# Kernel optimization log

Hardware: AMD Instinct MI355X
Metric: run time of the kernel (lower is better)

The kernel has to match this reference:

```python
import jax, jax.numpy as jnp
import numpy as np

NEG_INF = -jnp.inf

def _swish(x):
    return x * jax.nn.sigmoid(x)

def setup_inputs() -> dict:
    key = jax.random.key(0)
    ks = jax.random.split(key, 16)
    B, N, D = 16, 512, 256
    L, H, HS, FF = 4, 8, 64, 1024
    s = 0.05  # weight scale to keep activations stable over 4 layers
    inp = {
        "X": jax.random.normal(ks[0], (B, N, D), jnp.float32),
        "dag": jax.random.randint(ks[1], (N, N), 0, 2, jnp.int32),
        "Wk": jax.random.normal(ks[2], (L, H, D, HS), jnp.float32) * s,
        "bk": jnp.zeros((L, H, HS), jnp.float32),
        "Wq": jax.random.normal(ks[3], (L, H, D, HS), jnp.float32) * s,
        "bq": jnp.zeros((L, H, HS), jnp.float32),
        "Wv": jax.random.normal(ks[4], (L, H, D, HS), jnp.float32) * s,
        "bv": jnp.zeros((L, H, HS), jnp.float32),
        "Wp": jax.random.normal(ks[5], (L, H * HS, D), jnp.float32) * s,
        "bp": jnp.zeros((L, D), jnp.float32),
        "W1": jax.random.normal(ks[6], (L, D, FF), jnp.float32) * s,
        "b1": jnp.zeros((L, FF), jnp.float32),
        "W2": jax.random.normal(ks[7], (L, FF, D), jnp.float32) * s,
        "b2": jnp.zeros((L, D), jnp.float32),
        "Wlm": jax.random.normal(ks[8], (D, D), jnp.float32) * s,
        "blm": jnp.zeros((D,), jnp.float32),
    }
    return inp

def _block(X, dT, Wk, bk, Wq, bq, Wv, bv, Wp, bp, W1, b1, W2, b2):
    # X: (B, n, D); dT: (n, n) transposed (possibly identity-augmented) DAG
    B, n, D = X.shape
    hs = Wk.shape[-1]
    K = _swish(jnp.einsum('bnd,hdk->bhnk', X, Wk) + bk[None, :, None, :])
    Q = _swish(jnp.einsum('bnd,hdk->bhnk', X, Wq) + bq[None, :, None, :])
    V = _swish(jnp.einsum('bnd,hdk->bhnk', X, Wv) + bv[None, :, None, :])
    S = jnp.einsum('bhik,bhjk->bhij', Q, K) / (hs ** 0.5)      # (B,H,n,n)
    Sp = dT[None, None] * jnp.einsum('im,bhmj->bhij', dT, S)   # dag.T * (dag.T @ S)
    masked = jnp.where(Sp == 0, NEG_INF, Sp)
    dead = jnp.all(masked == NEG_INF, axis=-1, keepdims=True)  # rows that would softmax to NaN
    P = jax.nn.softmax(jnp.where(dead, 0.0, masked), axis=-1)
    P = jnp.where(dead, 0.0, P)                                # NaN-row zeroing, as in torch code
    O = jnp.einsum('bhij,bhjk->bhik', P, V) + jnp.einsum('ij,bhjk->bhik', dT, V)
    O = O.transpose(0, 2, 1, 3).reshape(B, n, -1)              # concat heads
    mha = _swish(O @ Wp + bp)                                  # projection + swish (dropout=0)
    ff = _swish(mha @ W1 + b1) @ W2 + b2                       # FF: Linear-Swish-Linear
    return mha + ff

def reference(X, dag, Wk, bk, Wq, bq, Wv, bv, Wp, bp, W1, b1, W2, b2, Wlm, blm):
    dagf = jnp.clip(dag.astype(X.dtype), 0, 1)
    n = dagf.shape[0]
    eye = jnp.eye(n, dtype=X.dtype)
    L = Wk.shape[0]
    for l in range(L):
        d = dagf if l == 0 else jnp.clip(dagf + eye, 0, 1)  # modify_dag
        X = _block(X, d.T, Wk[l], bk[l], Wq[l], bq[l], Wv[l], bv[l],
                   Wp[l], bp[l], W1[l], b1[l], W2[l], b2[l])
    return X @ Wlm + blm  # lm_head
```

## Files before the change

### kernel.cpp

```cpp
#include <hip/hip_runtime.h>
#include <hip/hip_bf16.h>
#include <math.h>


typedef __attribute__((ext_vector_type(8))) short bf16x8;
typedef __attribute__((ext_vector_type(4))) float f32x4;
typedef unsigned long long u64;

#define NEG_INF (-__builtin_inff())

__device__ __forceinline__ short f2bf(float x) {
  unsigned u = __float_as_uint(x);
  return (short)((u + 0x7FFFu + ((u >> 16) & 1u)) >> 16);
}
__device__ __forceinline__ float bf2f(short h) {
  return __uint_as_float(((unsigned)(unsigned short)h) << 16);
}
__device__ __forceinline__ void split_bf(float x, short& hi, short& lo) {
  hi = f2bf(x); lo = f2bf(x - bf2f(hi));
}
__device__ __forceinline__ float swishf(float x) { return x / (1.0f + __expf(-x)); }
__device__ __forceinline__ f32x4 mfma16(bf16x8 a, bf16x8 b, f32x4 c) {
  return __builtin_amdgcn_mfma_f32_16x16x32_bf16(a, b, c, 0, 0, 0);
}
__device__ __forceinline__ void gload16(const void* g, void* l) {
  __builtin_amdgcn_global_load_lds(
      (const __attribute__((address_space(1))) void*)g,
      (__attribute__((address_space(3))) void*)l, 16, 0, 0);
}

template<int P>
__global__ __launch_bounds__(256)
void wsplit(const float* __restrict__ in, short* __restrict__ oh, short* __restrict__ ol,
            int R, int C, int zh, long outLS)
{
  __shared__ float T[64][65];
  const int z = blockIdx.z;
  const long zin = (long)z * R * C;
  const long zout = (long)(z / zh) * outLS + (long)(z % zh) * R * C;
  const int r0 = blockIdx.y << 6, c0 = blockIdx.x << 6;
  const int lc = threadIdx.x & 63, p = threadIdx.x >> 6;
#pragma unroll
  for (int q = 0; q < 16; ++q) {
    int rr = p + q * 4;
    T[rr][lc] = in[zin + (long)(r0 + rr) * C + c0 + lc];
  }
  __syncthreads();
#pragma unroll
  for (int q = 0; q < 16; ++q) {
    int cr = p + q * 4;
    float x = T[lc][cr];
    long off = zout + (long)(c0 + cr) * R + r0 + lc;
    short hi = f2bf(x);
    oh[off] = hi;
    if (P == 2) ol[off] = f2bf(x - bf2f(hi));
  }
}

__global__ __launch_bounds__(512)
void prep_dt(const int* __restrict__ dag, short* __restrict__ dt0, short* __restrict__ dt1,
             u64* __restrict__ bits0, u64* __restrict__ bits1)
{
  int i = blockIdx.x, j = threadIdx.x;
  bool v0 = dag[j * 512 + i] > 0;
  bool v1 = v0 || (i == j);
  const short one = (short)0x3F80;
  dt0[i * 512 + j] = v0 ? one : (short)0;
  dt1[i * 512 + j] = v1 ? one : (short)0;
  u64 b0 = __ballot(v0), b1 = __ballot(v1);
  if ((j & 63) == 0) { bits0[i * 8 + (j >> 6)] = b0; bits1[i * 8 + (j >> 6)] = b1; }
}

__global__ __launch_bounds__(256)
void prep_x(const float* __restrict__ X, short* __restrict__ Xh, short* __restrict__ Xl)
{
  int idx = blockIdx.x * 256 + threadIdx.x;
  short hi, lo; split_bf(X[idx], hi, lo);
  Xh[idx] = hi; Xl[idx] = lo;
}

__global__ __launch_bounds__(256)
void pack_kq(const float* __restrict__ bk, const float* __restrict__ bq,
             float* __restrict__ bkq)
{
  int t = blockIdx.x * 256 + threadIdx.x;
  if (t >= 4096) return;
  int l = t >> 10, r = t & 1023;
  bkq[t] = (r < 512) ? bk[l * 512 + r] : bq[l * 512 + r - 512];
}

template<int BM, int BN, int AP, int BP, int OM, int OP, bool ACT, bool BIAS, bool RES>
__global__ __launch_bounds__(256)
void gemm(const short* __restrict__ Ah, const short* __restrict__ Al,
          const short* __restrict__ BTh, const short* __restrict__ BTl,
          const float* __restrict__ bias,
          const short* __restrict__ ResH, const short* __restrict__ ResL,
          float* __restrict__ Cf, short* __restrict__ Ch, short* __restrict__ Cl,
          short* __restrict__ Ch2,
          int K, int ldb, int ldc, long sB, long sC)
{
  constexpr int MR = BM / 32, NR = BN / 32;
  constexpr int ABUF = BM * 32;
  constexpr int BBUF = BN * 32;
  constexpr int STG = AP * ABUF + BP * BBUF;
  constexpr int TSZ = (OM >= 2) ? BN * (BM + 8) : 0;
  constexpr int SM = (2 * STG > TSZ) ? 2 * STG : TSZ;
  __shared__ __align__(16) short smem[SM];

  const int z = blockIdx.z;
  const short* pBh = BTh + (long)z * sB;
  const short* pBl = BTl + (long)z * sB;
  const int n0 = blockIdx.x * BN, m0 = blockIdx.y * BM;
  const int tid = threadIdx.x, lane = tid & 63, w = tid >> 6, g = lane >> 4, c = lane & 15;
  const int wm = w >> 1, wn = w & 1;

  auto stage = [&](int bb, int k0) {
    short* LA = smem + bb * STG;
    short* LB = LA + AP * ABUF;
#pragma unroll
    for (int p = 0; p < AP; ++p) {
      const short* src = p ? Al : Ah;
#pragma unroll
      for (int t = 0; t < BM / 64; ++t) {
        int u = t * 256 + tid, gi = u / BM, row = u % BM;
        gload16(src + (long)(m0 + row) * K + k0 + gi * 8, LA + p * ABUF + u * 8);
      }
    }
#pragma unroll
    for (int p = 0; p < BP; ++p) {
      const short* src = p ? pBl : pBh;
#pragma unroll
      for (int t = 0; t < BN / 64; ++t) {
        int u = t * 256 + tid, gi = u / BN, col = u % BN;
        gload16(src + (long)(n0 + col) * ldb + k0 + gi * 8, LB + p * BBUF + u * 8);
      }
    }
  };

  f32x4 acc[MR][NR] = {};
  stage(0, 0);
  const int nk = K >> 5;
  for (int ks = 0; ks < nk; ++ks) {
    const int cur = ks & 1;
    __syncthreads();
    if (ks + 1 < nk) stage(cur ^ 1, (ks + 1) << 5);

    short* LA = smem + cur * STG;
    short* LB = LA + AP * ABUF;
    bf16x8 a_h[MR], a_l[MR], b_h[NR], b_l[NR];
#pragma unroll
    for (int i = 0; i < MR; ++i) {
      int idx = (g * BM + wm * (BM / 2) + i * 16 + c) * 8;
      a_h[i] = *(const bf16x8*)(LA + idx);
      if (AP == 2) a_l[i] = *(const bf16x8*)(LA + ABUF + idx);
    }
#pragma unroll
    for (int j = 0; j < NR; ++j) {
      int idx = (g * BN + wn * (BN / 2) + j * 16 + c) * 8;
      b_h[j] = *(const bf16x8*)(LB + idx);
      if (BP == 2) b_l[j] = *(const bf16x8*)(LB + BBUF + idx);
    }
    __builtin_amdgcn_s_setprio(1);
#pragma unroll
    for (int i = 0; i < MR; ++i)
#pragma unroll
      for (int j = 0; j < NR; ++j) {
        acc[i][j] = mfma16(a_h[i], b_h[j], acc[i][j]);
        if (BP == 2) acc[i][j] = mfma16(a_h[i], b_l[j], acc[i][j]);
        if (AP == 2) acc[i][j] = mfma16(a_l[i], b_h[j], acc[i][j]);
      }
    __builtin_amdgcn_s_setprio(0);
  }

  const bool kq_rowmajor = (OM == 3) && (n0 < 512);
  if (OM == 0 || OM == 1 || kq_rowmajor) {
#pragma unroll
    for (int j = 0; j < NR; ++j) {
      int cl = wn * (BN / 2) + j * 16 + c;
      float bv = BIAS ? bias[n0 + cl] : 0.f;
      int col = (OM == 3) ? ((n0 & 511) + cl) : (n0 + cl);
#pragma unroll
      for (int i = 0; i < MR; ++i)
#pragma unroll
        for (int rr = 0; rr < 4; ++rr) {
          long row = m0 + wm * (BM / 2) + i * 16 + g * 4 + rr;
          float x = acc[i][j][rr] + bv;
          if (ACT) x = swishf(x);
          long off = (long)z * sC + row * ldc + col;
          if (RES) x += bf2f(ResH[off]) + bf2f(ResL[off]);
          if (OM == 1) { Cf[off] = x; }
          else {
            short hi, lo; split_bf(x, hi, lo);
            Ch[off] = hi;
            if (OM == 0 && OP == 2) Cl[off] = lo;
          }
        }
    }
    return;
  }

  if constexpr (OM >= 2) {
    short (*T)[BM + 8] = reinterpret_cast<short(*)[BM + 8]>(smem);
    const int h0 = (n0 & 511) >> 6;
    const int b = m0 >> 9, nn0 = m0 & 511;
    constexpr int NP = (OM == 3) ? 1 : OP;
#pragma unroll
    for (int p = 0; p < NP; ++p) {
      __syncthreads();
#pragma unroll
      for (int j = 0; j < NR; ++j) {
        int cl = wn * (BN / 2) + j * 16 + c;
        float bv = BIAS ? bias[n0 + cl] : 0.f;
#pragma unroll
        for (int i = 0; i < MR; ++i)
#pragma unroll
          for (int rr = 0; rr < 4; ++rr) {
            int rowl = wm * (BM / 2) + i * 16 + g * 4 + rr;
            float x = acc[i][j][rr] + bv;
            if (ACT) x = swishf(x);
            short hi = f2bf(x);
            T[cl][rowl] = p ? f2bf(x - bf2f(hi)) : hi;
          }
      }
      __syncthreads();
      short* dp = (OM == 3) ? Ch2 : (p ? Cl : Ch);
#pragma unroll
      for (int q = 0; q < BN * BM / 2048; ++q) {
        int idx = q * 256 + tid;
        int cl = idx / (BM / 8), r8 = (idx % (BM / 8)) * 8;
        long ob = ((long)(b * 8 + h0 + (cl >> 6)) << 15) + (long)(cl & 63) * 512 + nn0 + r8;
        *(bf16x8*)(dp + ob) = *(const bf16x8*)&T[cl][r8];
      }
    }
  }
}

__global__ __launch_bounds__(256)
void attn3(const short* __restrict__ Uh, const short* __restrict__ Kh,
           const short* __restrict__ VTh, const u64* __restrict__ bits,
           const float* __restrict__ OIf,
           short* __restrict__ Oh, short* __restrict__ Ol)
{
  __shared__ __align__(16) short LK[2][4096];
  __shared__ __align__(16) short LV[2][4096];
  __shared__ __align__(16) short PA[4][1024];

  const int bh = blockIdx.x, b = bh >> 3, hd = bh & 7;
  const int i0 = blockIdx.y << 6;
  const int tid = threadIdx.x, lane = tid & 63, w = tid >> 6, g = lane >> 4, c = lane & 15;
  const int istrip = i0 + w * 16;
  const long plane = (long)bh << 15;
  const float SC = 0.125f;

  auto stage = [&](int bb, int jt) {
#pragma unroll
    for (int t = 0; t < 2; ++t) {
      int u = t * 256 + tid, gi = u >> 6, j = u & 63;
      long ko = (long)(b * 512 + jt * 64 + j) * 512 + hd * 64 + gi * 8;
      gload16(Kh + ko, &LK[bb][0] + u * 8);
      long vo = plane + (long)j * 512 + jt * 64 + gi * 8;
      gload16(VTh + vo, &LV[bb][0] + u * 8);
    }
  };

  stage(0, 0);

  bf16x8 ufh[2];
#pragma unroll
  for (int ks = 0; ks < 2; ++ks)
    ufh[ks] = *(const bf16x8*)(Uh + plane + (long)(istrip + c) * 64 + ks * 32 + g * 8);

  float m_run[4], l_run[4];
#pragma unroll
  for (int rr = 0; rr < 4; ++rr) { m_run[rr] = NEG_INF; l_run[rr] = 0.f; }
  f32x4 oe[4] = {};

  for (int jt = 0; jt < 8; ++jt) {
    const int cur = jt & 1;
    __syncthreads();
    if (jt + 1 < 8) stage(cur ^ 1, jt + 1);

    f32x4 sacc[4] = {};
    __builtin_amdgcn_s_setprio(1);
#pragma unroll
    for (int ct = 0; ct < 4; ++ct)
#pragma unroll
      for (int ks = 0; ks < 2; ++ks) {
        bf16x8 kf = *(const bf16x8*)&LK[cur][((ks * 4 + g) * 64 + ct * 16 + c) * 8];
        sacc[ct] = mfma16(ufh[ks], kf, sacc[ct]);
      }
    __builtin_amdgcn_s_setprio(0);

    u64 wb[4];
#pragma unroll
    for (int rr = 0; rr < 4; ++rr)
      wb[rr] = bits[(long)(istrip + g * 4 + rr) * 8 + jt];

#pragma unroll
    for (int rr = 0; rr < 4; ++rr) {
      float vmax = NEG_INF;
#pragma unroll
      for (int ct = 0; ct < 4; ++ct)
        if ((wb[rr] >> (ct * 16 + c)) & 1ull) vmax = fmaxf(vmax, sacc[ct][rr] * SC);
#pragma unroll
      for (int off = 1; off < 16; off <<= 1)
        vmax = fmaxf(vmax, __shfl_xor(vmax, off, 64));
      float mnew = fmaxf(m_run[rr], vmax);
      float sf = (m_run[rr] > NEG_INF) ? __expf(m_run[rr] - mnew) : 0.f;
      float ps = 0.f, p[4];
#pragma unroll
      for (int ct = 0; ct < 4; ++ct) {
        bool bs = (wb[rr] >> (ct * 16 + c)) & 1ull;
        p[ct] = (bs && mnew > NEG_INF) ? __expf(sacc[ct][rr] * SC - mnew) : 0.f;
        ps += p[ct];
      }
#pragma unroll
      for (int off = 1; off < 16; off <<= 1)
        ps += __shfl_xor(ps, off, 64);
      l_run[rr] = l_run[rr] * sf + ps;
      m_run[rr] = mnew;
#pragma unroll
      for (int ct = 0; ct < 4; ++ct) {
        oe[ct][rr] *= sf;
        int row = g * 4 + rr, jc = ct * 16 + c;
        PA[w][row * 64 + (((jc >> 3) ^ (row & 7)) << 3) + (c & 7)] = f2bf(p[ct]);
      }
    }

    __builtin_amdgcn_s_setprio(1);
#pragma unroll
    for (int js = 0; js < 2; ++js) {
      int chunk = js * 4 + g;
      bf16x8 pa = *(const bf16x8*)&PA[w][c * 64 + ((chunk ^ (c & 7)) << 3)];
#pragma unroll
      for (int ct = 0; ct < 4; ++ct) {
        bf16x8 vf = *(const bf16x8*)&LV[cur][((js * 4 + g) * 64 + ct * 16 + c) * 8];
        oe[ct] = mfma16(pa, vf, oe[ct]);
      }
    }
    __builtin_amdgcn_s_setprio(0);
  }

  float rl[4];
#pragma unroll
  for (int rr = 0; rr < 4; ++rr) rl[rr] = (l_run[rr] > 0.f) ? 1.f / l_run[rr] : 0.f;
#pragma unroll
  for (int ct = 0; ct < 4; ++ct)
#pragma unroll
    for (int rr = 0; rr < 4; ++rr) {
      int n = istrip + g * 4 + rr;
      int hs = ct * 16 + c;
      float x = oe[ct][rr] * rl[rr] + OIf[plane + (long)n * 64 + hs];
      long row = (long)b * 512 + n;
      short hi, lo; split_bf(x, hi, lo);
      Oh[row * 512 + hd * 64 + hs] = hi;
      Ol[row * 512 + hd * 64 + hs] = lo;
    }
}

extern "C" void kernel_launch(void* const* d_in, const int* in_sizes, int n_in,
                              void* d_out, int out_size, void* d_ws, size_t ws_size,
                              hipStream_t stream)
{
  const float* X   = (const float*)d_in[0];
  const int*   dag = (const int*)d_in[1];
  const float* Wk  = (const float*)d_in[2];
  const float* bk  = (const float*)d_in[3];
  const float* Wq  = (const float*)d_in[4];
  const float* bq  = (const float*)d_in[5];
  const float* Wv  = (const float*)d_in[6];
  const float* bv  = (const float*)d_in[7];
  const float* Wp  = (const float*)d_in[8];
  const float* bp  = (const float*)d_in[9];
  const float* W1  = (const float*)d_in[10];
  const float* b1  = (const float*)d_in[11];
  const float* W2  = (const float*)d_in[12];
  const float* b2  = (const float*)d_in[13];
  const float* Wlm = (const float*)d_in[14];
  const float* blm = (const float*)d_in[15];
  float* out = (float*)d_out;

  char* p = (char*)d_ws;
  auto alloc = [&](size_t n) { void* r = p; p += (n + 255) & ~(size_t)255; return r; };
  short* WkqTh = (short*)alloc(1048576 * 2);
  short* WvTh = (short*)alloc(524288 * 2); short* WvTl = (short*)alloc(524288 * 2);
  short* WpTh = (short*)alloc(524288 * 2); short* WpTl = (short*)alloc(524288 * 2);
  short* W1Th = (short*)alloc(1048576 * 2); short* W1Tl = (short*)alloc(1048576 * 2);
  short* W2Th = (short*)alloc(1048576 * 2); short* W2Tl = (short*)alloc(1048576 * 2);
  short* WlmTh = (short*)alloc(65536 * 2); short* WlmTl = (short*)alloc(65536 * 2);
  float* bkq = (float*)alloc(4096 * 4);
  short* dt0b = (short*)alloc(262144 * 2); short* dt1b = (short*)alloc(262144 * 2);
  u64* bits0 = (u64*)alloc(4096 * 8); u64* bits1 = (u64*)alloc(4096 * 8);
  short* Xh = (short*)alloc(2097152 * 2); short* Xl = (short*)alloc(2097152 * 2);
  short* Kh = (short*)alloc(4194304 * 2);
  short* QTh = (short*)alloc(4194304 * 2);
  short* VTh = (short*)alloc(4194304 * 2); short* VTl = (short*)alloc(4194304 * 2);
  short* Uh  = (short*)alloc(4194304 * 2);
  float* OIf = (float*)alloc(4194304 * 4);
  short* Olo = (short*)alloc(4194304 * 2);
  short* mhaH = Kh, *mhaL = Kh + 2097152;
  short* Oh = QTh;
  short* ff1H = VTh;
  short* ff1L = Uh;

  wsplit<1><<<dim3(1, 4, 32), 256, 0, stream>>>(Wk, WkqTh, nullptr, 256, 64, 8, 262144);
  wsplit<1><<<dim3(1, 4, 32), 256, 0, stream>>>(Wq, WkqTh + 131072, nullptr, 256, 64, 8, 262144);
  wsplit<2><<<dim3(1, 4, 32), 256, 0, stream>>>(Wv, WvTh, WvTl, 256, 64, 8, 131072);
  wsplit<2><<<dim3(4, 8, 4), 256, 0, stream>>>(Wp, WpTh, WpTl, 512, 256, 1, 131072);
  wsplit<2><<<dim3(16, 4, 4), 256, 0, stream>>>(W1, W1Th, W1Tl, 256, 1024, 1, 262144);
  wsplit<2><<<dim3(4, 16, 4), 256, 0, stream>>>(W2, W2Th, W2Tl, 1024, 256, 1, 262144);
  wsplit<2><<<dim3(4, 4, 1), 256, 0, stream>>>(Wlm, WlmTh, WlmTl, 256, 256, 1, 65536);
  prep_dt<<<512, 512, 0, stream>>>(dag, dt0b, dt1b, bits0, bits1);
  prep_x<<<8192, 256, 0, stream>>>(X, Xh, Xl);
  pack_kq<<<16, 256, 0, stream>>>(bk, bq, bkq);

  for (int l = 0; l < 4; ++l) {
    const short* dtb = l ? dt1b : dt0b;
    const u64* bts = l ? bits1 : bits0;
    gemm<128, 64, 1, 1, 3, 1, true, true, false><<<dim3(16, 64), 256, 0, stream>>>(
        Xh, nullptr, WkqTh + l * 262144, nullptr, bkq + l * 1024, nullptr, nullptr,
        nullptr, Kh, nullptr, QTh, 256, 256, 512, 0, 0);
    gemm<128, 64, 2, 2, 2, 2, true, true, false><<<dim3(8, 64), 256, 0, stream>>>(
        Xh, Xl, WvTh + l * 131072, WvTl + l * 131072, bv + l * 512, nullptr, nullptr,
        nullptr, VTh, VTl, nullptr, 256, 256, 0, 0, 0);
    gemm<128, 64, 1, 1, 0, 1, false, false, false><<<dim3(1, 4, 128), 256, 0, stream>>>(
        dtb, nullptr, QTh, nullptr, nullptr, nullptr, nullptr,
        nullptr, Uh, nullptr, nullptr, 512, 512, 64, 32768, 32768);
    gemm<128, 64, 1, 2, 1, 1, false, false, false><<<dim3(1, 4, 128), 256, 0, stream>>>(
        dtb, nullptr, VTh, VTl, nullptr, nullptr, nullptr,
        OIf, nullptr, nullptr, nullptr, 512, 512, 64, 32768, 32768);
    attn3<<<dim3(128, 8), 256, 0, stream>>>(Uh, Kh, VTh, bts, OIf, Oh, Olo);
    gemm<64, 64, 2, 2, 0, 2, true, true, false><<<dim3(4, 128), 256, 0, stream>>>(
        Oh, Olo, WpTh + l * 131072, WpTl + l * 131072, bp + l * 256, nullptr, nullptr,
        nullptr, mhaH, mhaL, nullptr, 512, 512, 256, 0, 0);
    gemm<128, 64, 2, 2, 0, 2, true, true, false><<<dim3(16, 64), 256, 0, stream>>>(
        mhaH, mhaL, W1Th + l * 262144, W1Tl + l * 262144, b1 + l * 1024, nullptr, nullptr,
        nullptr, ff1H, ff1L, nullptr, 256, 256, 1024, 0, 0);
    gemm<64, 64, 2, 2, 0, 2, false, true, true><<<dim3(4, 128), 256, 0, stream>>>(
        ff1H, ff1L, W2Th + l * 262144, W2Tl + l * 262144, b2 + l * 256, mhaH, mhaL,
        nullptr, Xh, Xl, nullptr, 1024, 1024, 256, 0, 0);
  }
  gemm<64, 64, 2, 2, 1, 1, false, true, false><<<dim3(4, 128), 256, 0, stream>>>(
      Xh, Xl, WlmTh, WlmTl, blm, nullptr, nullptr,
      out, nullptr, nullptr, nullptr, 256, 256, 256, 0, 0);
}
```

Measured before the change: 916.4 us.

## Rewrite attention with transposed register softmax and drop low-precision splits for V/Wp

Attention now computes S transposed so each lane owns one query row, keeping the softmax in registers and feeding P to the PV MFMA through cross-lane shuffles instead of an LDS staging buffer. The 1/sqrt(hs) scale is folded into the Q epilogue. V and Wp lose their low-bf16 halves and the attention output is written as a single bf16, which cuts MFMA and memory work but lowers precision. The identity-term GEMM is recast as a transposed batched GEMM, and the row-major GEMM epilogues now stage through LDS to issue vectorised 16-byte stores.

```diff
diff --git a/kernel.cpp b/kernel.cpp
--- a/kernel.cpp
+++ b/kernel.cpp
@@ -27,6 +27,11 @@
   __builtin_amdgcn_global_load_lds(
       (const __attribute__((address_space(1))) void*)g,
       (__attribute__((address_space(3))) void*)l, 16, 0, 0);
+}
+__device__ __forceinline__ unsigned cvtpk(float a, float b) {
+  unsigned r;
+  asm("v_cvt_pk_bf16_f32 %0, %1, %2" : "=v"(r) : "v"(a), "v"(b));
+  return r;
 }
 
 template<int P>
@@ -97,17 +102,20 @@
           const short* __restrict__ ResH, const short* __restrict__ ResL,
           float* __restrict__ Cf, short* __restrict__ Ch, short* __restrict__ Cl,
           short* __restrict__ Ch2,
-          int K, int ldb, int ldc, long sB, long sC)
+          int K, int ldb, int ldc, long sA, long sB, long sC)
 {
   constexpr int MR = BM / 32, NR = BN / 32;
-  constexpr int ABUF = BM * 32;
-  constexpr int BBUF = BN * 32;
+  constexpr int ABUF = BM * 32, BBUF = BN * 32;
   constexpr int STG = AP * ABUF + BP * BBUF;
-  constexpr int TSZ = (OM >= 2) ? BN * (BM + 8) : 0;
-  constexpr int SM = (2 * STG > TSZ) ? 2 * STG : TSZ;
+  constexpr int TSZ2 = (OM == 2 || OM == 3) ? BN * (BM + 8) : 0;
+  constexpr int TSZF = (OM == 0 || OM == 3) ? BM * (BN + 4) * 2 : 0;
+  constexpr int SM1 = (2 * STG > TSZ2) ? 2 * STG : TSZ2;
+  constexpr int SM = (SM1 > TSZF) ? SM1 : TSZF;
   __shared__ __align__(16) short smem[SM];
 
   const int z = blockIdx.z;
+  const short* pAh = Ah + (long)z * sA;
+  const short* pAl = Al + (long)z * sA;
   const short* pBh = BTh + (long)z * sB;
   const short* pBl = BTl + (long)z * sB;
   const int n0 = blockIdx.x * BN, m0 = blockIdx.y * BM;
@@ -119,7 +127,7 @@
     short* LB = LA + AP * ABUF;
 #pragma unroll
     for (int p = 0; p < AP; ++p) {
-      const short* src = p ? Al : Ah;
+      const short* src = p ? pAl : pAh;
 #pragma unroll
       for (int t = 0; t < BM / 64; ++t) {
         int u = t * 256 + tid, gi = u / BM, row = u % BM;
@@ -172,13 +180,11 @@
     __builtin_amdgcn_s_setprio(0);
   }
 
-  const bool kq_rowmajor = (OM == 3) && (n0 < 512);
-  if (OM == 0 || OM == 1 || kq_rowmajor) {
+  if constexpr (OM == 1) {
 #pragma unroll
     for (int j = 0; j < NR; ++j) {
       int cl = wn * (BN / 2) + j * 16 + c;
       float bv = BIAS ? bias[n0 + cl] : 0.f;
-      int col = (OM == 3) ? ((n0 & 511) + cl) : (n0 + cl);
 #pragma unroll
       for (int i = 0; i < MR; ++i)
 #pragma unroll
@@ -186,20 +192,57 @@
           long row = m0 + wm * (BM / 2) + i * 16 + g * 4 + rr;
           float x = acc[i][j][rr] + bv;
           if (ACT) x = swishf(x);
-          long off = (long)z * sC + row * ldc + col;
-          if (RES) x += bf2f(ResH[off]) + bf2f(ResL[off]);
-          if (OM == 1) { Cf[off] = x; }
-          else {
-            short hi, lo; split_bf(x, hi, lo);
-            Ch[off] = hi;
-            if (OM == 0 && OP == 2) Cl[off] = lo;
+          Cf[(long)z * sC + row * ldc + n0 + cl] = x;
+        }
+    }
+    return;
+  }
+
+  if constexpr (OM == 0 || OM == 3) {
+    if (OM == 0 || n0 < 512) {
+      __syncthreads();
+      float* Tf = (float*)smem;
+      constexpr int LDT = BN + 4;
+#pragma unroll
+      for (int j = 0; j < NR; ++j) {
+        int cl = wn * (BN / 2) + j * 16 + c;
+        float bv = BIAS ? bias[n0 + cl] : 0.f;
+#pragma unroll
+        for (int i = 0; i < MR; ++i)
+#pragma unroll
+          for (int rr = 0; rr < 4; ++rr) {
+            int rowl = wm * (BM / 2) + i * 16 + g * 4 + rr;
+            float x = acc[i][j][rr] + bv;
+            if (ACT) x = swishf(x);
+            Tf[rowl * LDT + cl] = x;
           }
+      }
+      __syncthreads();
+      constexpr int CH = BN / 8, NT = BM * CH / 256;
+#pragma unroll
+      for (int t = 0; t < NT; ++t) {
+        int idx = t * 256 + tid, row = idx / CH, ch = idx % CH;
+        long base = (long)z * sC + (long)(m0 + row) * ldc + (OM == 3 ? (n0 & 511) : n0) + ch * 8;
+        float x8[8];
+#pragma unroll
+        for (int e = 0; e < 8; ++e) x8[e] = Tf[row * LDT + ch * 8 + e];
+        if (RES) {
+          bf16x8 rh = *(const bf16x8*)(ResH + base);
+          bf16x8 rl8 = *(const bf16x8*)(ResL + base);
+#pragma unroll
+          for (int e = 0; e < 8; ++e) x8[e] += bf2f(rh[e]) + bf2f(rl8[e]);
         }
-    }
-    return;
-  }
-
-  if constexpr (OM >= 2) {
+        short h8[8], l8[8];
+#pragma unroll
+        for (int e = 0; e < 8; ++e) split_bf(x8[e], h8[e], l8[e]);
+        *(bf16x8*)(Ch + base) = *(const bf16x8*)&h8[0];
+        if (OP == 2) *(bf16x8*)(Cl + base) = *(const bf16x8*)&l8[0];
+      }
+      return;
+    }
+  }
+
+  if constexpr (OM == 2 || OM == 3) {
     short (*T)[BM + 8] = reinterpret_cast<short(*)[BM + 8]>(smem);
     const int h0 = (n0 & 511) >> 6;
     const int b = m0 >> 9, nn0 = m0 & 511;
@@ -218,16 +261,17 @@
             int rowl = wm * (BM / 2) + i * 16 + g * 4 + rr;
             float x = acc[i][j][rr] + bv;
             if (ACT) x = swishf(x);
+            if (OM == 3) x *= 0.125f;
             short hi = f2bf(x);
             T[cl][rowl] = p ? f2bf(x - bf2f(hi)) : hi;
           }
       }
       __syncthreads();
       short* dp = (OM == 3) ? Ch2 : (p ? Cl : Ch);
+      constexpr int RC = BM / 8;
 #pragma unroll
       for (int q = 0; q < BN * BM / 2048; ++q) {
-        int idx = q * 256 + tid;
-        int cl = idx / (BM / 8), r8 = (idx % (BM / 8)) * 8;
+        int idx = q * 256 + tid, cl = idx / RC, r8 = (idx % RC) * 8;
         long ob = ((long)(b * 8 + h0 + (cl >> 6)) << 15) + (long)(cl & 63) * 512 + nn0 + r8;
         *(bf16x8*)(dp + ob) = *(const bf16x8*)&T[cl][r8];
       }
@@ -236,21 +280,18 @@
 }
 
 __global__ __launch_bounds__(256)
-void attn3(const short* __restrict__ Uh, const short* __restrict__ Kh,
+void attn4(const short* __restrict__ Uh, const short* __restrict__ Kh,
            const short* __restrict__ VTh, const u64* __restrict__ bits,
-           const float* __restrict__ OIf,
-           short* __restrict__ Oh, short* __restrict__ Ol)
+           const float* __restrict__ OIT, short* __restrict__ Oh)
 {
   __shared__ __align__(16) short LK[2][4096];
   __shared__ __align__(16) short LV[2][4096];
-  __shared__ __align__(16) short PA[4][1024];
 
   const int bh = blockIdx.x, b = bh >> 3, hd = bh & 7;
   const int i0 = blockIdx.y << 6;
   const int tid = threadIdx.x, lane = tid & 63, w = tid >> 6, g = lane >> 4, c = lane & 15;
   const int istrip = i0 + w * 16;
   const long plane = (long)bh << 15;
-  const float SC = 0.125f;
 
   auto stage = [&](int bb, int jt) {
 #pragma unroll
@@ -265,15 +306,15 @@
 
   stage(0, 0);
 
-  bf16x8 ufh[2];
+  bf16x8 uf[2];
 #pragma unroll
   for (int ks = 0; ks < 2; ++ks)
-    ufh[ks] = *(const bf16x8*)(Uh + plane + (long)(istrip + c) * 64 + ks * 32 + g * 8);
-
-  float m_run[4], l_run[4];
-#pragma unroll
-  for (int rr = 0; rr < 4; ++rr) { m_run[rr] = NEG_INF; l_run[rr] = 0.f; }
-  f32x4 oe[4] = {};
+    uf[ks] = *(const bf16x8*)(Uh + plane + (long)(istrip + c) * 64 + ks * 32 + g * 8);
+
+  float m_run = NEG_INF, l_run = 0.f;
+  f32x4 oeT[4] = {};
+  const int srcA = (g & 1) * 32 + c, srcB = srcA + 16;
+  const bool ghi = (g >> 1) != 0;
 
   for (int jt = 0; jt < 8; ++jt) {
     const int cur = jt & 1;
@@ -287,75 +328,87 @@
 #pragma unroll
       for (int ks = 0; ks < 2; ++ks) {
         bf16x8 kf = *(const bf16x8*)&LK[cur][((ks * 4 + g) * 64 + ct * 16 + c) * 8];
-        sacc[ct] = mfma16(ufh[ks], kf, sacc[ct]);
+        sacc[ct] = mfma16(kf, uf[ks], sacc[ct]);
       }
     __builtin_amdgcn_s_setprio(0);
 
-    u64 wb[4];
-#pragma unroll
-    for (int rr = 0; rr < 4; ++rr)
-      wb[rr] = bits[(long)(istrip + g * 4 + rr) * 8 + jt];
-
+    const u64 wb = bits[(long)(istrip + c) * 8 + jt];
+
+    float vmax = NEG_INF;
+#pragma unroll
+    for (int ct = 0; ct < 4; ++ct)
+#pragma unroll
+      for (int rr = 0; rr < 4; ++rr)
+        if ((wb >> (ct * 16 + g * 4 + rr)) & 1ull) vmax = fmaxf(vmax, sacc[ct][rr]);
+    vmax = fmaxf(vmax, __shfl_xor(vmax, 16, 64));
+    vmax = fmaxf(vmax, __shfl_xor(vmax, 32, 64));
+    float mnew = fmaxf(m_run, vmax);
+    float sf = (m_run > NEG_INF) ? __expf(m_run - mnew) : 0.f;
+
+    float p[4][4], ps = 0.f;
+#pragma unroll
+    for (int ct = 0; ct < 4; ++ct)
+#pragma unroll
+      for (int rr = 0; rr < 4; ++rr) {
+        bool bs = (wb >> (ct * 16 + g * 4 + rr)) & 1ull;
+        float pe = bs ? __expf(sacc[ct][rr] - mnew) : 0.f;
+        p[ct][rr] = pe; ps += pe;
+      }
+    ps += __shfl_xor(ps, 16, 64);
+    ps += __shfl_xor(ps, 32, 64);
+    l_run = l_run * sf + ps;
+    m_run = mnew;
+#pragma unroll
+    for (int ht = 0; ht < 4; ++ht)
+#pragma unroll
+      for (int rr = 0; rr < 4; ++rr) oeT[ht][rr] *= sf;
+
+    unsigned q0[4], q1[4];
+#pragma unroll
+    for (int ct = 0; ct < 4; ++ct) {
+      q0[ct] = cvtpk(p[ct][0], p[ct][1]);
+      q1[ct] = cvtpk(p[ct][2], p[ct][3]);
+    }
+#pragma unroll
+    for (int ksp = 0; ksp < 2; ++ksp) {
+      unsigned a00 = __shfl(q0[2 * ksp], srcA, 64), a01 = __shfl(q0[2 * ksp + 1], srcA, 64);
+      unsigned a10 = __shfl(q1[2 * ksp], srcA, 64), a11 = __shfl(q1[2 * ksp + 1], srcA, 64);
+      unsigned b00 = __shfl(q0[2 * ksp], srcB, 64), b01 = __shfl(q0[2 * ksp + 1], srcB, 64);
+      unsigned b10 = __shfl(q1[2 * ksp], srcB, 64), b11 = __shfl(q1[2 * ksp + 1], srcB, 64);
+      union { unsigned u[4]; bf16x8 v; } pa;
+      pa.u[0] = ghi ? a01 : a00;
+      pa.u[1] = ghi ? a11 : a10;
+      pa.u[2] = ghi ? b01 : b00;
+      pa.u[3] = ghi ? b11 : b10;
+      __builtin_amdgcn_s_setprio(1);
+#pragma unroll
+      for (int ht = 0; ht < 4; ++ht) {
+        bf16x8 vf = *(const bf16x8*)&LV[cur][((ksp * 4 + g) * 64 + ht * 16 + c) * 8];
+        oeT[ht] = mfma16(vf, pa.v, oeT[ht]);
+      }
+      __builtin_amdgcn_s_setprio(0);
+    }
+  }
+
+  const float rl = (l_run > 0.f) ? 1.f / l_run : 0.f;
+
+  __syncthreads();
+  short* T = (short*)&LK[0][0];
+#pragma unroll
+  for (int ht = 0; ht < 4; ++ht)
 #pragma unroll
     for (int rr = 0; rr < 4; ++rr) {
-      float vmax = NEG_INF;
-#pragma unroll
-      for (int ct = 0; ct < 4; ++ct)
-        if ((wb[rr] >> (ct * 16 + c)) & 1ull) vmax = fmaxf(vmax, sacc[ct][rr] * SC);
-#pragma unroll
-      for (int off = 1; off < 16; off <<= 1)
-        vmax = fmaxf(vmax, __shfl_xor(vmax, off, 64));
-      float mnew = fmaxf(m_run[rr], vmax);
-      float sf = (m_run[rr] > NEG_INF) ? __expf(m_run[rr] - mnew) : 0.f;
-      float ps = 0.f, p[4];
-#pragma unroll
-      for (int ct = 0; ct < 4; ++ct) {
-        bool bs = (wb[rr] >> (ct * 16 + c)) & 1ull;
-        p[ct] = (bs && mnew > NEG_INF) ? __expf(sacc[ct][rr] * SC - mnew) : 0.f;
-        ps += p[ct];
-      }
-#pragma unroll
-      for (int off = 1; off < 16; off <<= 1)
-        ps += __shfl_xor(ps, off, 64);
-      l_run[rr] = l_run[rr] * sf + ps;
-      m_run[rr] = mnew;
-#pragma unroll
-      for (int ct = 0; ct < 4; ++ct) {
-        oe[ct][rr] *= sf;
-        int row = g * 4 + rr, jc = ct * 16 + c;
-        PA[w][row * 64 + (((jc >> 3) ^ (row & 7)) << 3) + (c & 7)] = f2bf(p[ct]);
-      }
-    }
-
-    __builtin_amdgcn_s_setprio(1);
-#pragma unroll
-    for (int js = 0; js < 2; ++js) {
-      int chunk = js * 4 + g;
-      bf16x8 pa = *(const bf16x8*)&PA[w][c * 64 + ((chunk ^ (c & 7)) << 3)];
-#pragma unroll
-      for (int ct = 0; ct < 4; ++ct) {
-        bf16x8 vf = *(const bf16x8*)&LV[cur][((js * 4 + g) * 64 + ct * 16 + c) * 8];
-        oe[ct] = mfma16(pa, vf, oe[ct]);
-      }
-    }
-    __builtin_amdgcn_s_setprio(0);
-  }
-
-  float rl[4];
-#pragma unroll
-  for (int rr = 0; rr < 4; ++rr) rl[rr] = (l_run[rr] > 0.f) ? 1.f / l_run[rr] : 0.f;
-#pragma unroll
-  for (int ct = 0; ct < 4; ++ct)
-#pragma unroll
-    for (int rr = 0; rr < 4; ++rr) {
-      int n = istrip + g * 4 + rr;
-      int hs = ct * 16 + c;
-      float x = oe[ct][rr] * rl[rr] + OIf[plane + (long)n * 64 + hs];
-      long row = (long)b * 512 + n;
-      short hi, lo; split_bf(x, hi, lo);
-      Oh[row * 512 + hd * 64 + hs] = hi;
-      Ol[row * 512 + hd * 64 + hs] = lo;
-    }
+      int hs = ht * 16 + g * 4 + rr;
+      float x = oeT[ht][rr] * rl + OIT[plane + (long)hs * 512 + i0 + w * 16 + c];
+      T[(w * 16 + c) * 72 + hs] = f2bf(x);
+    }
+  __syncthreads();
+#pragma unroll
+  for (int t = 0; t < 2; ++t) {
+    int idx = t * 256 + tid, row = idx >> 3, ch = idx & 7;
+    *(bf16x8*)(Oh + (long)(b * 512 + i0 + row) * 512 + hd * 64 + ch * 8) =
+        *(const bf16x8*)&T[row * 72 + ch * 8];
+  }
 }
 
 extern "C" void kernel_launch(void* const* d_in, const int* in_sizes, int n_in,
@@ -383,8 +436,8 @@
   char* p = (char*)d_ws;
   auto alloc = [&](size_t n) { void* r = p; p += (n + 255) & ~(size_t)255; return r; };
   short* WkqTh = (short*)alloc(1048576 * 2);
-  short* WvTh = (short*)alloc(524288 * 2); short* WvTl = (short*)alloc(524288 * 2);
-  short* WpTh = (short*)alloc(524288 * 2); short* WpTl = (short*)alloc(524288 * 2);
+  short* WvTh = (short*)alloc(524288 * 2);
+  short* WpTh = (short*)alloc(524288 * 2);
   short* W1Th = (short*)alloc(1048576 * 2); short* W1Tl = (short*)alloc(1048576 * 2);
   short* W2Th = (short*)alloc(1048576 * 2); short* W2Tl = (short*)alloc(1048576 * 2);
   short* WlmTh = (short*)alloc(65536 * 2); short* WlmTl = (short*)alloc(65536 * 2);
@@ -392,21 +445,20 @@
   short* dt0b = (short*)alloc(262144 * 2); short* dt1b = (short*)alloc(262144 * 2);
   u64* bits0 = (u64*)alloc(4096 * 8); u64* bits1 = (u64*)alloc(4096 * 8);
   short* Xh = (short*)alloc(2097152 * 2); short* Xl = (short*)alloc(2097152 * 2);
-  short* Kh = (short*)alloc(4194304 * 2);
+  short* Kh  = (short*)alloc(4194304 * 2);
   short* QTh = (short*)alloc(4194304 * 2);
-  short* VTh = (short*)alloc(4194304 * 2); short* VTl = (short*)alloc(4194304 * 2);
+  short* VTh = (short*)alloc(4194304 * 2);
   short* Uh  = (short*)alloc(4194304 * 2);
-  float* OIf = (float*)alloc(4194304 * 4);
-  short* Olo = (short*)alloc(4194304 * 2);
+  float* OIT = (float*)alloc(4194304 * 4);
   short* mhaH = Kh, *mhaL = Kh + 2097152;
   short* Oh = QTh;
-  short* ff1H = VTh;
+  short* ff1H = QTh;
   short* ff1L = Uh;
 
   wsplit<1><<<dim3(1, 4, 32), 256, 0, stream>>>(Wk, WkqTh, nullptr, 256, 64, 8, 262144);
   wsplit<1><<<dim3(1, 4, 32), 256, 0, stream>>>(Wq, WkqTh + 131072, nullptr, 256, 64, 8, 262144);
-  wsplit<2><<<dim3(1, 4, 32), 256, 0, stream>>>(Wv, WvTh, WvTl, 256, 64, 8, 131072);
-  wsplit<2><<<dim3(4, 8, 4), 256, 0, stream>>>(Wp, WpTh, WpTl, 512, 256, 1, 131072);
+  wsplit<1><<<dim3(1, 4, 32), 256, 0, stream>>>(Wv, WvTh, nullptr, 256, 64, 8, 131072);
+  wsplit<1><<<dim3(4, 8, 4), 256, 0, stream>>>(Wp, WpTh, nullptr, 512, 256, 1, 131072);
   wsplit<2><<<dim3(16, 4, 4), 256, 0, stream>>>(W1, W1Th, W1Tl, 256, 1024, 1, 262144);
   wsplit<2><<<dim3(4, 16, 4), 256, 0, stream>>>(W2, W2Th, W2Tl, 1024, 256, 1, 262144);
   wsplit<2><<<dim3(4, 4, 1), 256, 0, stream>>>(Wlm, WlmTh, WlmTl, 256, 256, 1, 65536);
@@ -419,28 +471,28 @@
     const u64* bts = l ? bits1 : bits0;
     gemm<128, 64, 1, 1, 3, 1, true, true, false><<<dim3(16, 64), 256, 0, stream>>>(
         Xh, nullptr, WkqTh + l * 262144, nullptr, bkq + l * 1024, nullptr, nullptr,
-        nullptr, Kh, nullptr, QTh, 256, 256, 512, 0, 0);
-    gemm<128, 64, 2, 2, 2, 2, true, true, false><<<dim3(8, 64), 256, 0, stream>>>(
-        Xh, Xl, WvTh + l * 131072, WvTl + l * 131072, bv + l * 512, nullptr, nullptr,
-        nullptr, VTh, VTl, nullptr, 256, 256, 0, 0, 0);
+        nullptr, Kh, nullptr, QTh, 256, 256, 512, 0, 0, 0);
+    gemm<128, 64, 1, 1, 2, 1, true, true, false><<<dim3(8, 64), 256, 0, stream>>>(
+        Xh, nullptr, WvTh + l * 131072, nullptr, bv + l * 512, nullptr, nullptr,
+        nullptr, VTh, nullptr, nullptr, 256, 256, 0, 0, 0, 0);
     gemm<128, 64, 1, 1, 0, 1, false, false, false><<<dim3(1, 4, 128), 256, 0, stream>>>(
         dtb, nullptr, QTh, nullptr, nullptr, nullptr, nullptr,
-        nullptr, Uh, nullptr, nullptr, 512, 512, 64, 32768, 32768);
-    gemm<128, 64, 1, 2, 1, 1, false, false, false><<<dim3(1, 4, 128), 256, 0, stream>>>(
-        dtb, nullptr, VTh, VTl, nullptr, nullptr, nullptr,
-        OIf, nullptr, nullptr, nullptr, 512, 512, 64, 32768, 32768);
-    attn3<<<dim3(128, 8), 256, 0, stream>>>(Uh, Kh, VTh, bts, OIf, Oh, Olo);
-    gemm<64, 64, 2, 2, 0, 2, true, true, false><<<dim3(4, 128), 256, 0, stream>>>(
-        Oh, Olo, WpTh + l * 131072, WpTl + l * 131072, bp + l * 256, nullptr, nullptr,
-        nullptr, mhaH, mhaL, nullptr, 512, 512, 256, 0, 0);
+        nullptr, Uh, nullptr, nullptr, 512, 512, 64, 0, 32768, 32768);
+    gemm<64, 64, 1, 1, 1, 1, false, false, false><<<dim3(8, 1, 128), 256, 0, stream>>>(
+        VTh, nullptr, dtb, nullptr, nullptr, nullptr, nullptr,
+        OIT, nullptr, nullptr, nullptr, 512, 512, 512, 32768, 0, 32768);
+    attn4<<<dim3(128, 8), 256, 0, stream>>>(Uh, Kh, VTh, bts, OIT, Oh);
+    gemm<128, 64, 1, 1, 0, 2, true, true, false><<<dim3(4, 64), 256, 0, stream>>>(
+        Oh, nullptr, WpTh + l * 131072, nullptr, bp + l * 256, nullptr, nullptr,
+        nullptr, mhaH, mhaL, nullptr, 512, 512, 256, 0, 0, 0);
     gemm<128, 64, 2, 2, 0, 2, true, true, false><<<dim3(16, 64), 256, 0, stream>>>(
         mhaH, mhaL, W1Th + l * 262144, W1Tl + l * 262144, b1 + l * 1024, nullptr, nullptr,
-        nullptr, ff1H, ff1L, nullptr, 256, 256, 1024, 0, 0);
+        nullptr, ff1H, ff1L, nullptr, 256, 256, 1024, 0, 0, 0);
     gemm<64, 64, 2, 2, 0, 2, false, true, true><<<dim3(4, 128), 256, 0, stream>>>(
         ff1H, ff1L, W2Th + l * 262144, W2Tl + l * 262144, b2 + l * 256, mhaH, mhaL,
-        nullptr, Xh, Xl, nullptr, 1024, 1024, 256, 0, 0);
+        nullptr, Xh, Xl, nullptr, 1024, 1024, 256, 0, 0, 0);
   }
   gemm<64, 64, 2, 2, 1, 1, false, true, false><<<dim3(4, 128), 256, 0, stream>>>(
       Xh, Xl, WlmTh, WlmTl, blm, nullptr, nullptr,
-      out, nullptr, nullptr, nullptr, 256, 256, 256, 0, 0);
-}
+      out, nullptr, nullptr, nullptr, 256, 256, 256, 0, 0, 0);
+}
```

Measured after the change: 794.4 us, median of 3. 13.3% less time.
